# Kernel optimization log

Measured on AMD Instinct MI355X. Metric: run time of the kernel, lower is better.

Reference implementation:

```python
import jax, jax.numpy as jnp
import numpy as np

B, N, D = 8, 2048, 256

def setup_inputs() -> dict:
    key = jax.random.key(0)
    ks = jax.random.split(key, 8)
    sc = 1.0 / np.sqrt(D)
    return {
        "x": jax.random.normal(ks[0], (B, N, D), dtype=jnp.float32),
        "W_fp": jax.random.normal(ks[1], (D, D), dtype=jnp.float32) * sc,
        "b_fp": jnp.zeros((D,), dtype=jnp.float32),
        "w_s": jax.random.normal(ks[2], (D,), dtype=jnp.float32) * sc,
        "b_s": jnp.zeros((), dtype=jnp.float32),
        "W_rp": jax.random.normal(ks[3], (D, D), dtype=jnp.float32) * sc,
        "b_rp": jnp.zeros((D,), dtype=jnp.float32),
        "W_gp": jax.random.normal(ks[4], (D, D), dtype=jnp.float32) * sc,
        "b_gp": jnp.zeros((D,), dtype=jnp.float32),
        "gamma": jnp.ones((D,), dtype=jnp.float32),
        "beta": jnp.zeros((D,), dtype=jnp.float32),
    }

def reference(x, W_fp, b_fp, w_s, b_s, W_rp, b_rp, W_gp, b_gp, gamma, beta):
    # feature projection: [B, N, D]
    proj = jnp.einsum('bnd,de->bne', x, W_fp) + b_fp
    # F.normalize(p=2, dim=-1) with eps=1e-12
    nrm = jnp.sqrt(jnp.sum(proj * proj, axis=-1, keepdims=True))
    xn = proj / jnp.maximum(nrm, 1e-12)
    # cosine similarity matrix [B, N, N]
    sim = jnp.einsum('bnd,bmd->bnm', xn, xn)
    # adj_scaler: Linear(D,1)+sigmoid is constant along the broadcast axis ->
    # compute per-node scalar once [B, N] (same math as the O(N^2*D) expand)
    s = jax.nn.sigmoid(jnp.einsum('bnd,d->bn', proj, w_s) + b_s)
    scaler = jnp.clip(0.5 * (s[:, :, None] + s[:, None, :]), 1e-6, 1.0)
    adj = jnp.maximum(scaler * sim, 1e-6)  # clamp(min=1e-6)
    degree = jnp.maximum(jnp.sum(adj, axis=2, keepdims=True), 1e-6)
    norm_adj = adj / degree
    # aggregation + region projection
    region = jnp.einsum('bnm,bmd->bnd', norm_adj, proj)
    region = jnp.einsum('bnd,de->bne', region, W_rp) + b_rp
    # global pooling + projection: [B, 1, D]
    g = jnp.mean(region, axis=1, keepdims=True)
    g = jnp.einsum('bnd,de->bne', g, W_gp) + b_gp
    input_global = jnp.mean(x, axis=1, keepdims=True)
    h = g + input_global
    # LayerNorm (eps=1e-5)
    mu = jnp.mean(h, axis=-1, keepdims=True)
    var = jnp.mean((h - mu) ** 2, axis=-1, keepdims=True)
    out = (h - mu) / jnp.sqrt(var + 1e-5) * gamma + beta
    return out, adj
```

## Files before the change

kernel.cpp:

```cpp
#include <hip/hip_runtime.h>
#include <hip/hip_bf16.h>
#include <math.h>

#define Bn 8
#define Nn 2048
#define Dn 256

typedef short short8 __attribute__((ext_vector_type(8)));
typedef float floatx4 __attribute__((ext_vector_type(4)));

__device__ __forceinline__ short f2bf_bits(float f) {
    __bf16 h = (__bf16)f;
    return __builtin_bit_cast(short, h);
}

__device__ __forceinline__ float bf2f(short s) {
    unsigned u = ((unsigned)(unsigned short)s) << 16;
    return __builtin_bit_cast(float, u);
}

__device__ __forceinline__ void gl_lds16(const void* gsrc, void* ldst) {
    __builtin_amdgcn_global_load_lds(
        (const __attribute__((address_space(1))) void*)gsrc,
        (__attribute__((address_space(3))) void*)ldst, 16, 0, 0);
}

__device__ __forceinline__ float sigmoidf_(float z) {
    return 1.0f / (1.0f + __expf(-z));
}


__global__ void k_transpose(const float* __restrict__ W, short* __restrict__ Wt) {
    int e = blockIdx.x, d = threadIdx.x;
    Wt[e * Dn + d] = f2bf_bits(W[d * Dn + e]);
}


__global__ __launch_bounds__(256) void k_projxn(
    const float* __restrict__ x, const short* __restrict__ Wt,
    const float* __restrict__ b_fp, const float* __restrict__ w_s,
    short* __restrict__ xn, float* __restrict__ sdot, float* __restrict__ nrm,
    float* __restrict__ xpart) {
    __shared__ __align__(16) short As[64 * 64];
    __shared__ __align__(16) short Bs[256 * 64];
    __shared__ float xsumS[4 * 256];
    const int t = threadIdx.x;
    const int bm = blockIdx.x * 64;
    const int lane = t & 63, wv = t >> 6;
    const int wm = wv * 16;
    const int l15 = lane & 15, q = lane >> 4;

    for (int i = t; i < 1024; i += 256) xsumS[i] = 0.f;

    floatx4 acc[16];
    #pragma unroll
    for (int j = 0; j < 16; ++j) acc[j] = (floatx4){0.f, 0.f, 0.f, 0.f};

    const int rA = t >> 2, cA = (t & 3) * 16;
    const int rB = t >> 3, cB = (t & 7) * 8;

    for (int k0 = 0; k0 < Dn; k0 += 64) {
        const float* gp = x + (size_t)(bm + rA) * Dn + k0 + cA;
        float4 v0 = *(const float4*)gp;
        float4 v1 = *(const float4*)(gp + 4);
        float4 v2 = *(const float4*)(gp + 8);
        float4 v3 = *(const float4*)(gp + 12);
        short8 o0, o1;
        o0[0] = f2bf_bits(v0.x); o0[1] = f2bf_bits(v0.y);
        o0[2] = f2bf_bits(v0.z); o0[3] = f2bf_bits(v0.w);
        o0[4] = f2bf_bits(v1.x); o0[5] = f2bf_bits(v1.y);
        o0[6] = f2bf_bits(v1.z); o0[7] = f2bf_bits(v1.w);
        o1[0] = f2bf_bits(v2.x); o1[1] = f2bf_bits(v2.y);
        o1[2] = f2bf_bits(v2.z); o1[3] = f2bf_bits(v2.w);
        o1[4] = f2bf_bits(v3.x); o1[5] = f2bf_bits(v3.y);
        o1[6] = f2bf_bits(v3.z); o1[7] = f2bf_bits(v3.w);
        *(short8*)(As + rA * 64 + cA) = o0;
        *(short8*)(As + rA * 64 + cA + 8) = o1;
        #pragma unroll
        for (int cc = 0; cc < 8; ++cc)
            gl_lds16(Wt + (size_t)(cc * 32 + rB) * Dn + k0 + cB,
                     Bs + (cc * 32 + rB) * 64 + cB);
        __syncthreads();
        #pragma unroll
        for (int ks = 0; ks < 2; ++ks) {
            short8 af = *(const short8*)(As + (wm + l15) * 64 + ks * 32 + q * 8);
            #pragma unroll
            for (int j = 0; j < 16; ++j) {
                short8 bfr = *(const short8*)(Bs + (j * 16 + l15) * 64 + ks * 32 + q * 8);
                acc[j] = __builtin_amdgcn_mfma_f32_16x16x32_bf16(af, bfr, acc[j], 0, 0, 0);
            }
        }
        {
            float s = 0.f;
            #pragma unroll
            for (int r = 0; r < 16; ++r)
                s += bf2f(As[(wm + r) * 64 + lane]);
            xsumS[wv * 256 + k0 + lane] += s;
        }
        __syncthreads();
    }
    {
        float xs = xsumS[t] + xsumS[256 + t] + xsumS[512 + t] + xsumS[768 + t];
        xpart[(size_t)blockIdx.x * Dn + t] = xs;
    }
    float bfv[16], wsv[16];
    #pragma unroll
    for (int j = 0; j < 16; ++j) {
        bfv[j] = b_fp[j * 16 + l15];
        wsv[j] = w_s[j * 16 + l15];
    }
    #pragma unroll
    for (int reg = 0; reg < 4; ++reg) {
        int row = bm + wm + q * 4 + reg;
        float v[16];
        float pw = 0.f, pn = 0.f;
        #pragma unroll
        for (int j = 0; j < 16; ++j) {
            v[j] = acc[j][reg] + bfv[j];
            pw += v[j] * wsv[j];
            pn += v[j] * v[j];
        }
        #pragma unroll
        for (int m = 1; m < 16; m <<= 1) {
            pw += __shfl_xor(pw, m);
            pn += __shfl_xor(pn, m);
        }
        float nc = fmaxf(sqrtf(pn), 1e-12f);
        float inv = 1.0f / nc;
        size_t rbase = (size_t)row * Dn + l15;
        #pragma unroll
        for (int j = 0; j < 16; ++j)
            xn[rbase + j * 16] = f2bf_bits(v[j] * inv);
        if (l15 == 0) {
            sdot[row] = pw;
            nrm[row] = nc;
        }
    }
}


__global__ __launch_bounds__(256) void k_sim(
    const short* __restrict__ xn, const float* __restrict__ sdot,
    const float* __restrict__ b_s, float* __restrict__ adj,
    float* __restrict__ deg_part) {
    __shared__ __align__(16) short As[128 * 64];
    __shared__ __align__(16) short Bs[128 * 64];
    __shared__ float degS[2][128];
    const int t = threadIdx.x;
    const int cx = blockIdx.x;
    const int bn = cx * 128;
    const int bm = blockIdx.y * 128;
    const int b = blockIdx.z;
    const int lane = t & 63, wv = t >> 6;
    const int wm = (wv >> 1) * 64, wn = (wv & 1) * 64;
    const int l15 = lane & 15, q = lane >> 4;
    const int rr = t >> 3, c8 = (t & 7) * 8;
    const short* xb = xn + (size_t)b * Nn * Dn;

    floatx4 acc[4][4];
    #pragma unroll
    for (int i = 0; i < 4; ++i)
        #pragma unroll
        for (int j = 0; j < 4; ++j) acc[i][j] = (floatx4){0.f, 0.f, 0.f, 0.f};

    for (int k0 = 0; k0 < Dn; k0 += 64) {
        #pragma unroll
        for (int cc = 0; cc < 4; ++cc) {
            int r = cc * 32 + rr;
            gl_lds16(xb + (size_t)(bm + r) * Dn + k0 + c8, As + r * 64 + c8);
            gl_lds16(xb + (size_t)(bn + r) * Dn + k0 + c8, Bs + r * 64 + c8);
        }
        __syncthreads();
        #pragma unroll
        for (int ks = 0; ks < 2; ++ks) {
            short8 af[4], bfr[4];
            #pragma unroll
            for (int i = 0; i < 4; ++i)
                af[i] = *(const short8*)(As + (wm + i * 16 + l15) * 64 + ks * 32 + q * 8);
            #pragma unroll
            for (int j = 0; j < 4; ++j)
                bfr[j] = *(const short8*)(Bs + (wn + j * 16 + l15) * 64 + ks * 32 + q * 8);
            #pragma unroll
            for (int i = 0; i < 4; ++i)
                #pragma unroll
                for (int j = 0; j < 4; ++j)
                    acc[i][j] = __builtin_amdgcn_mfma_f32_16x16x32_bf16(af[i], bfr[j], acc[i][j], 0, 0, 0);
        }
        __syncthreads();
    }
    const float bsv = b_s[0];
    float scol[4];
    #pragma unroll
    for (int j = 0; j < 4; ++j)
        scol[j] = sigmoidf_(sdot[b * Nn + bn + wn + j * 16 + l15] + bsv);
    #pragma unroll
    for (int i = 0; i < 4; ++i) {
        #pragma unroll
        for (int reg = 0; reg < 4; ++reg) {
            int lr = wm + i * 16 + q * 4 + reg;
            int row = bm + lr;
            float srow = sigmoidf_(sdot[b * Nn + row] + bsv);
            size_t obase = ((size_t)b * Nn + row) * Nn + bn + wn + l15;
            float rs = 0.f;
            #pragma unroll
            for (int j = 0; j < 4; ++j) {
                float sc = 0.5f * (srow + scol[j]);
                sc = fminf(fmaxf(sc, 1e-6f), 1.0f);
                float v = fmaxf(sc * acc[i][j][reg], 1e-6f);
                adj[obase + (size_t)j * 16] = v;
                rs += v;
            }
            #pragma unroll
            for (int m = 1; m < 16; m <<= 1) rs += __shfl_xor(rs, m);
            if (l15 == 0) degS[wv & 1][lr] = rs;
        }
    }
    __syncthreads();
    if (t < 128)
        deg_part[((size_t)(b * 16 + cx)) * Nn + bm + t] = degS[0][t] + degS[1][t];
}


__global__ __launch_bounds__(512) void k_colsum(
    const float* __restrict__ adj, const float* __restrict__ deg_part,
    const short* __restrict__ xn, const float* __restrict__ nrm,
    float* __restrict__ gpart) {
    int b = blockIdx.x, ck = blockIdx.y, t = threadIdx.x;
    __shared__ float invdeg[Nn];
    __shared__ float part[32][64];
    __shared__ float csL[64];
    #pragma unroll
    for (int rc = 0; rc < 4; ++rc) {
        int row = rc * 512 + t;
        float s = 0.f;
        #pragma unroll
        for (int cx = 0; cx < 16; ++cx)
            s += deg_part[((size_t)(b * 16 + cx)) * Nn + row];
        invdeg[row] = 1.0f / fmaxf(s, 1e-6f);
    }
    __syncthreads();
    const int lc = (t & 15) * 4;
    const int rg = t >> 4;
    const int c0 = ck * 64;
    float sx = 0.f, sy = 0.f, sz = 0.f, sw = 0.f;
    for (int r = rg; r < Nn; r += 32) {
        float4 v = *(const float4*)(adj + ((size_t)b * Nn + r) * Nn + c0 + lc);
        float w = invdeg[r];
        sx += v.x * w; sy += v.y * w; sz += v.z * w; sw += v.w * w;
    }
    part[rg][lc + 0] = sx; part[rg][lc + 1] = sy;
    part[rg][lc + 2] = sz; part[rg][lc + 3] = sw;
    __syncthreads();
    if (t < 64) {
        float s = 0.f;
        #pragma unroll
        for (int g = 0; g < 32; ++g) s += part[g][t];
        csL[t] = s * nrm[b * Nn + c0 + t];
    }
    __syncthreads();
    if (t < Dn) {
        float g = 0.f;
        #pragma unroll 4
        for (int m = 0; m < 64; ++m)
            g += csL[m] * bf2f(xn[((size_t)(b * Nn + c0 + m)) * Dn + t]);
        gpart[(b * 32 + ck) * Dn + t] = g;
    }
}


__global__ __launch_bounds__(256) void k_final2(
    const float* __restrict__ gpart, const float* __restrict__ xpart,
    const float* __restrict__ W_rp, const float* __restrict__ b_rp,
    const float* __restrict__ W_gp, const float* __restrict__ b_gp,
    const float* __restrict__ gamma, const float* __restrict__ beta,
    float* __restrict__ out) {
    int b = blockIdx.x, t = threadIdx.x;
    __shared__ float gp_s[Dn];
    __shared__ float g1_s[Dn];
    __shared__ float red[8];
    float gs = 0.f, xs = 0.f;
    #pragma unroll
    for (int ck = 0; ck < 32; ++ck) {
        gs += gpart[(b * 32 + ck) * Dn + t];
        xs += xpart[(b * 32 + ck) * Dn + t];
    }
    gp_s[t] = gs * (1.0f / Nn);
    float xm = xs * (1.0f / Nn);
    __syncthreads();
    float g1 = b_rp[t];
    #pragma unroll 4
    for (int d = 0; d < Dn; ++d) g1 += gp_s[d] * W_rp[d * Dn + t];
    g1_s[t] = g1;
    __syncthreads();
    float g2 = b_gp[t];
    #pragma unroll 4
    for (int e = 0; e < Dn; ++e) g2 += g1_s[e] * W_gp[e * Dn + t];
    float h = g2 + xm;
    float sum = h;
    #pragma unroll
    for (int m = 1; m < 64; m <<= 1) sum += __shfl_xor(sum, m);
    if ((t & 63) == 0) red[t >> 6] = sum;
    __syncthreads();
    float mu = (red[0] + red[1] + red[2] + red[3]) * (1.0f / Dn);
    float dv = h - mu;
    float s2 = dv * dv;
    #pragma unroll
    for (int m = 1; m < 64; m <<= 1) s2 += __shfl_xor(s2, m);
    if ((t & 63) == 0) red[4 + (t >> 6)] = s2;
    __syncthreads();
    float var = (red[4] + red[5] + red[6] + red[7]) * (1.0f / Dn);
    out[b * Dn + t] = dv * rsqrtf(var + 1e-5f) * gamma[t] + beta[t];
}


extern "C" void kernel_launch(void* const* d_in, const int* in_sizes, int n_in,
                              void* d_out, int out_size, void* d_ws, size_t ws_size,
                              hipStream_t stream) {
    const float* x     = (const float*)d_in[0];
    const float* W_fp  = (const float*)d_in[1];
    const float* b_fp  = (const float*)d_in[2];
    const float* w_s   = (const float*)d_in[3];
    const float* b_s   = (const float*)d_in[4];
    const float* W_rp  = (const float*)d_in[5];
    const float* b_rp  = (const float*)d_in[6];
    const float* W_gp  = (const float*)d_in[7];
    const float* b_gp  = (const float*)d_in[8];
    const float* gamma = (const float*)d_in[9];
    const float* beta  = (const float*)d_in[10];

    float* out = (float*)d_out;
    float* adj = out + Bn * Dn;

    char* ws = (char*)d_ws;
    short* xn    = (short*)(ws);
    short* Wt    = (short*)(ws + 8388608);
    float* sdot  = (float*)(ws + 8519680);
    float* nrm   = (float*)(ws + 8585216);
    float* degp  = (float*)(ws + 8650752);
    float* gpart = (float*)(ws + 9699328);
    float* xpart = (float*)(ws + 9961472);

    k_transpose<<<Dn, Dn, 0, stream>>>(W_fp, Wt);
    k_projxn<<<(Bn * Nn) / 64, 256, 0, stream>>>(x, Wt, b_fp, w_s, xn, sdot, nrm, xpart);
    k_sim<<<dim3(Nn / 128, Nn / 128, Bn), 256, 0, stream>>>(xn, sdot, b_s, adj, degp);
    k_colsum<<<dim3(Bn, 32), 512, 0, stream>>>(adj, degp, xn, nrm, gpart);
    k_final2<<<Bn, 256, 0, stream>>>(gpart, xpart, W_rp, b_rp, W_gp, b_gp, gamma, beta, out);
}
```

Before: 289.7 us.

## Transpose MFMA operands for float4 adj stores, remap grid batch-innermost, split colsum dot

The sim kernel swaps the MFMA A/B operands so each lane holds four consecutive columns of one row. The 128MB adj matrix can then be written with float4 stores instead of scalar strided stores, and the row-sum reduction needs two shuffles instead of four. Block indices are linearised so the batch index varies fastest, which changes how tiles spread across XCDs and caches. The colsum kernel splits its final 64-row dot product across all 512 threads and combines the two halves through shared memory.

```diff
diff --git a/kernel.cpp b/kernel.cpp
--- a/kernel.cpp
+++ b/kernel.cpp
@@ -147,13 +147,15 @@
     __shared__ __align__(16) short Bs[128 * 64];
     __shared__ float degS[2][128];
     const int t = threadIdx.x;
-    const int cx = blockIdx.x;
+    int lin = (blockIdx.z * 16 + blockIdx.y) * 16 + blockIdx.x;
+    const int b = lin & 7;
+    const int pos = lin >> 3;
+    const int by = pos >> 4, cx = pos & 15;
     const int bn = cx * 128;
-    const int bm = blockIdx.y * 128;
-    const int b = blockIdx.z;
+    const int bm = by * 128;
     const int lane = t & 63, wv = t >> 6;
     const int wm = (wv >> 1) * 64, wn = (wv & 1) * 64;
-    const int l15 = lane & 15, q = lane >> 4;
+    const int l15 = lane & 15, q4 = lane >> 4;
     const int rr = t >> 3, c8 = (t & 7) * 8;
     const short* xb = xn + (size_t)b * Nn * Dn;
 
@@ -176,44 +178,51 @@
             short8 af[4], bfr[4];
             #pragma unroll
             for (int i = 0; i < 4; ++i)
-                af[i] = *(const short8*)(As + (wm + i * 16 + l15) * 64 + ks * 32 + q * 8);
+                af[i] = *(const short8*)(As + (wm + i * 16 + l15) * 64 + ks * 32 + q4 * 8);
             #pragma unroll
             for (int j = 0; j < 4; ++j)
-                bfr[j] = *(const short8*)(Bs + (wn + j * 16 + l15) * 64 + ks * 32 + q * 8);
+                bfr[j] = *(const short8*)(Bs + (wn + j * 16 + l15) * 64 + ks * 32 + q4 * 8);
             #pragma unroll
             for (int i = 0; i < 4; ++i)
                 #pragma unroll
                 for (int j = 0; j < 4; ++j)
-                    acc[i][j] = __builtin_amdgcn_mfma_f32_16x16x32_bf16(af[i], bfr[j], acc[i][j], 0, 0, 0);
+                    acc[i][j] = __builtin_amdgcn_mfma_f32_16x16x32_bf16(bfr[j], af[i], acc[i][j], 0, 0, 0);
         }
         __syncthreads();
     }
     const float bsv = b_s[0];
-    float scol[4];
+    float srow[4];
+    #pragma unroll
+    for (int i = 0; i < 4; ++i)
+        srow[i] = sigmoidf_(sdot[b * Nn + bm + wm + i * 16 + l15] + bsv);
+    float scol[4][4];
     #pragma unroll
     for (int j = 0; j < 4; ++j)
-        scol[j] = sigmoidf_(sdot[b * Nn + bn + wn + j * 16 + l15] + bsv);
+        #pragma unroll
+        for (int reg = 0; reg < 4; ++reg)
+            scol[j][reg] = sigmoidf_(sdot[b * Nn + bn + wn + j * 16 + q4 * 4 + reg] + bsv);
     #pragma unroll
     for (int i = 0; i < 4; ++i) {
-        #pragma unroll
-        for (int reg = 0; reg < 4; ++reg) {
-            int lr = wm + i * 16 + q * 4 + reg;
-            int row = bm + lr;
-            float srow = sigmoidf_(sdot[b * Nn + row] + bsv);
-            size_t obase = ((size_t)b * Nn + row) * Nn + bn + wn + l15;
-            float rs = 0.f;
-            #pragma unroll
-            for (int j = 0; j < 4; ++j) {
-                float sc = 0.5f * (srow + scol[j]);
-                sc = fminf(fmaxf(sc, 1e-6f), 1.0f);
-                float v = fmaxf(sc * acc[i][j][reg], 1e-6f);
-                adj[obase + (size_t)j * 16] = v;
-                rs += v;
-            }
-            #pragma unroll
-            for (int m = 1; m < 16; m <<= 1) rs += __shfl_xor(rs, m);
-            if (l15 == 0) degS[wv & 1][lr] = rs;
-        }
+        float rs = 0.f;
+        size_t rbase = ((size_t)b * Nn + (bm + wm + i * 16 + l15)) * Nn + bn + wn + q4 * 4;
+        #pragma unroll
+        for (int j = 0; j < 4; ++j) {
+            float4 o;
+            float sc;
+            sc = fminf(fmaxf(0.5f * (srow[i] + scol[j][0]), 1e-6f), 1.0f);
+            o.x = fmaxf(sc * acc[i][j][0], 1e-6f);
+            sc = fminf(fmaxf(0.5f * (srow[i] + scol[j][1]), 1e-6f), 1.0f);
+            o.y = fmaxf(sc * acc[i][j][1], 1e-6f);
+            sc = fminf(fmaxf(0.5f * (srow[i] + scol[j][2]), 1e-6f), 1.0f);
+            o.z = fmaxf(sc * acc[i][j][2], 1e-6f);
+            sc = fminf(fmaxf(0.5f * (srow[i] + scol[j][3]), 1e-6f), 1.0f);
+            o.w = fmaxf(sc * acc[i][j][3], 1e-6f);
+            *(float4*)(adj + rbase + (size_t)j * 16) = o;
+            rs += o.x + o.y + o.z + o.w;
+        }
+        rs += __shfl_xor(rs, 16);
+        rs += __shfl_xor(rs, 32);
+        if (q4 == 0) degS[wv & 1][wm + i * 16 + l15] = rs;
     }
     __syncthreads();
     if (t < 128)
@@ -229,6 +238,7 @@
     __shared__ float invdeg[Nn];
     __shared__ float part[32][64];
     __shared__ float csL[64];
+    __shared__ float gHalf[2][Dn];
     #pragma unroll
     for (int rc = 0; rc < 4; ++rc) {
         int row = rc * 512 + t;
@@ -258,13 +268,19 @@
         csL[t] = s * nrm[b * Nn + c0 + t];
     }
     __syncthreads();
-    if (t < Dn) {
+    {
+        int h = t >> 8, d = t & 255;
         float g = 0.f;
         #pragma unroll 4
-        for (int m = 0; m < 64; ++m)
-            g += csL[m] * bf2f(xn[((size_t)(b * Nn + c0 + m)) * Dn + t]);
-        gpart[(b * 32 + ck) * Dn + t] = g;
-    }
+        for (int mi = 0; mi < 32; ++mi) {
+            int m = h * 32 + mi;
+            g += csL[m] * bf2f(xn[((size_t)(b * Nn + c0 + m)) * Dn + d]);
+        }
+        gHalf[h][d] = g;
+    }
+    __syncthreads();
+    if (t < Dn)
+        gpart[(b * 32 + ck) * Dn + t] = gHalf[0][t] + gHalf[1][t];
 }
 
 
```

New measurement: 280.3 us. 3.2% less time.
